# Optimization experiments

Measured on AMD Instinct MI355X. Metric: run time of the kernel, lower is better.

## Reference

```python
import jax, jax.numpy as jnp
import numpy as np

NUM_NODES = 500_000
NUM_EDGES = 8_000_000
NUM_GRAPHS = 8_192


def gcn_conv(x, edge_index, W, b):
    """PyG GCNConv (default args): add self-loops, symmetric deg normalization.
    Messages flow source (row=edge_index[0]) -> target (col=edge_index[1])."""
    n = x.shape[0]
    loop = jnp.arange(n, dtype=edge_index.dtype)
    row = jnp.concatenate([edge_index[0], loop])
    col = jnp.concatenate([edge_index[1], loop])
    h = x @ W  # [n, out]
    deg = jax.ops.segment_sum(jnp.ones_like(col, dtype=x.dtype), col, num_segments=n)
    dinv = jnp.where(deg > 0, jax.lax.rsqrt(deg), 0.0)
    norm = dinv[row] * dinv[col]  # [E+n]
    msg = h[row] * norm[:, None]  # gather + scale
    out = jax.ops.segment_sum(msg, col, num_segments=n)  # scatter-add at targets
    return out + b


def global_mean_pool(x, batch, num_graphs):
    s = jax.ops.segment_sum(x, batch, num_segments=num_graphs)
    cnt = jax.ops.segment_sum(jnp.ones((x.shape[0],), dtype=x.dtype), batch, num_segments=num_graphs)
    return s / jnp.maximum(cnt, 1.0)[:, None]


def setup_inputs() -> dict:
    key = jax.random.key(0)
    ks = jax.random.split(key, 12)
    x = jax.random.normal(ks[0], (NUM_NODES, 9), dtype=jnp.float32)
    edge_index = jax.random.randint(ks[1], (2, NUM_EDGES), 0, NUM_NODES, dtype=jnp.int64)
    batch = jnp.sort(jax.random.randint(ks[2], (NUM_NODES,), 0, NUM_GRAPHS, dtype=jnp.int64))
    metadata = jax.random.normal(ks[3], (NUM_GRAPHS, 27), dtype=jnp.float32)
    def glorot(k, shape):
        lim = float(np.sqrt(6.0 / (shape[0] + shape[1])))
        return jax.random.uniform(k, shape, jnp.float32, -lim, lim)
    W1 = glorot(ks[4], (9, 16));  b1 = jnp.zeros((16,), jnp.float32)
    W2 = glorot(ks[5], (16, 16)); b2 = jnp.zeros((16,), jnp.float32)
    Wh1 = glorot(ks[6], (16 + 27, 16)); bh1 = jnp.zeros((16,), jnp.float32)
    Wh2 = glorot(ks[7], (16, 1));       bh2 = jnp.zeros((1,), jnp.float32)
    return {"x": x, "edge_index": edge_index, "batch": batch, "metadata": metadata,
            "W1": W1, "b1": b1, "W2": W2, "b2": b2,
            "Wh1": Wh1, "bh1": bh1, "Wh2": Wh2, "bh2": bh2}


def reference(x, edge_index, batch, metadata, W1, b1, W2, b2, Wh1, bh1, Wh2, bh2):
    # eval mode: dropout is identity
    h = jax.nn.relu(gcn_conv(x, edge_index, W1, b1))
    h = jax.nn.relu(gcn_conv(h, edge_index, W2, b2))
    emb = global_mean_pool(h, batch, metadata.shape[0])  # [G, 16]
    z = jnp.concatenate([emb, metadata], axis=1)          # [G, 43]
    z = jax.nn.relu(z @ Wh1 + bh1)
    return z @ Wh2 + bh2  # [G, 1]
```

## Files before the change

### kernel.cpp

```cpp
#include <hip/hip_runtime.h>
#include <hip/hip_fp8.h>

#define N_NODES 500000
#define N_EDGES 8000000
#define N_GRAPHS 8192
#define BKT 512
#define NBK 977
#define C_CAP 9216
#define TILE2 8192
#define NTB2 977
#define CSR_IT 9

typedef __attribute__((ext_vector_type(2))) float v2f;

#if __has_builtin(__builtin_amdgcn_cvt_pk_f32_fp8)
template <bool HI>
__device__ __forceinline__ v2f cvt2fp8(unsigned w) {
    return __builtin_amdgcn_cvt_pk_f32_fp8((int)w, HI);
}
#else
template <bool HI>
__device__ __forceinline__ v2f cvt2fp8(unsigned w) {
    unsigned h16 = HI ? (w >> 16) : (w & 0xFFFFu);
    __hip_fp8_e4m3 a, b;
    a.__x = (__hip_fp8_storage_t)(h16 & 0xFFu);
    b.__x = (__hip_fp8_storage_t)(h16 >> 8);
    v2f r; r.x = (float)a; r.y = (float)b; return r;
}
#endif
#if __has_builtin(__builtin_amdgcn_cvt_pk_fp8_f32)
__device__ __forceinline__ unsigned pk4fp8(float a, float b, float c, float d) {
    int r = 0;
    r = __builtin_amdgcn_cvt_pk_fp8_f32(a, b, r, false);
    r = __builtin_amdgcn_cvt_pk_fp8_f32(c, d, r, true);
    return (unsigned)r;
}
#else
__device__ __forceinline__ unsigned pk4fp8(float a, float b, float c, float d) {
    __hip_fp8_e4m3 qa(a), qb(b), qc(c), qd(d);
    return (unsigned)qa.__x | ((unsigned)qb.__x << 8) |
           ((unsigned)qc.__x << 16) | ((unsigned)qd.__x << 24);
}
#endif
__device__ __forceinline__ void addfp8x16(float* acc, uint4 a) {
    v2f p;
    p = cvt2fp8<false>(a.x); acc[0] += p.x; acc[1] += p.y;
    p = cvt2fp8<true>(a.x);  acc[2] += p.x; acc[3] += p.y;
    p = cvt2fp8<false>(a.y); acc[4] += p.x; acc[5] += p.y;
    p = cvt2fp8<true>(a.y);  acc[6] += p.x; acc[7] += p.y;
    p = cvt2fp8<false>(a.z); acc[8] += p.x; acc[9] += p.y;
    p = cvt2fp8<true>(a.z);  acc[10] += p.x; acc[11] += p.y;
    p = cvt2fp8<false>(a.w); acc[12] += p.x; acc[13] += p.y;
    p = cvt2fp8<true>(a.w);  acc[14] += p.x; acc[15] += p.y;
}
__device__ __forceinline__ void addfp8x8(float* acc, uint2 a) {
    v2f p;
    p = cvt2fp8<false>(a.x); acc[0] += p.x; acc[1] += p.y;
    p = cvt2fp8<true>(a.x);  acc[2] += p.x; acc[3] += p.y;
    p = cvt2fp8<false>(a.y); acc[4] += p.x; acc[5] += p.y;
    p = cvt2fp8<true>(a.y);  acc[6] += p.x; acc[7] += p.y;
}

__global__ void k_init(float* __restrict__ pooled, int* __restrict__ gcursor) {
    int i = blockIdx.x * 256 + threadIdx.x;
    if (i < N_GRAPHS * 17) pooled[i] = 0.0f;
    if (i < NBK) gcursor[i] = i * C_CAP;
}

__global__ __launch_bounds__(1024) void
k_build(const int4* __restrict__ row4, const int4* __restrict__ col4,
        int* __restrict__ gcursor, unsigned* __restrict__ packed, int E) {
    __shared__ unsigned sortedv[TILE2];
    __shared__ unsigned short sortedb[TILE2];
    __shared__ int hist2[2][1024];
    __shared__ int lbase[1024];
    __shared__ int runbase[1024];
    __shared__ int sd[1024];
    int t = threadIdx.x, b = blockIdx.x;
    int sub = t >> 9;
    hist2[0][t] = 0; hist2[1][t] = 0;
    __syncthreads();
    unsigned uval[8];
    unsigned short ub[8];
#pragma unroll
    for (int k = 0; k < 2; k++) {
        int vi = b * 2048 + k * 1024 + t;
        int j0 = k * 4;
        if (vi * 4 < E) {
            int4 c = col4[vi];
            int4 r = row4[vi];
            unsigned cc, rr;
            cc = (unsigned)c.x; rr = (unsigned)r.x;
            if (cc < N_NODES && rr < N_NODES) { uval[j0] = (rr << 9) | (cc & 511u); ub[j0] = (unsigned short)(cc >> 9); atomicAdd(&hist2[sub][cc >> 9], 1); } else ub[j0] = 0xFFFFu;
            cc = (unsigned)c.y; rr = (unsigned)r.y;
            if (cc < N_NODES && rr < N_NODES) { uval[j0+1] = (rr << 9) | (cc & 511u); ub[j0+1] = (unsigned short)(cc >> 9); atomicAdd(&hist2[sub][cc >> 9], 1); } else ub[j0+1] = 0xFFFFu;
            cc = (unsigned)c.z; rr = (unsigned)r.z;
            if (cc < N_NODES && rr < N_NODES) { uval[j0+2] = (rr << 9) | (cc & 511u); ub[j0+2] = (unsigned short)(cc >> 9); atomicAdd(&hist2[sub][cc >> 9], 1); } else ub[j0+2] = 0xFFFFu;
            cc = (unsigned)c.w; rr = (unsigned)r.w;
            if (cc < N_NODES && rr < N_NODES) { uval[j0+3] = (rr << 9) | (cc & 511u); ub[j0+3] = (unsigned short)(cc >> 9); atomicAdd(&hist2[sub][cc >> 9], 1); } else ub[j0+3] = 0xFFFFu;
        } else {
            ub[j0] = 0xFFFFu; ub[j0+1] = 0xFFFFu; ub[j0+2] = 0xFFFFu; ub[j0+3] = 0xFFFFu;
        }
    }
    __syncthreads();
    int tot = (t < NBK) ? (hist2[0][t] + hist2[1][t]) : 0;
    sd[t] = tot; __syncthreads();
    for (int d = 1; d < 1024; d <<= 1) {
        int tv = (t >= d) ? sd[t - d] : 0;
        __syncthreads(); sd[t] += tv; __syncthreads();
    }
    lbase[t] = sd[t] - tot;
    if (t < NBK && tot) runbase[t] = atomicAdd(&gcursor[t], tot);
    hist2[0][t] = 0;
    __syncthreads();
    int total = sd[1023];
#pragma unroll
    for (int j = 0; j < 8; j++) {
        unsigned bb = ub[j];
        if (bb != 0xFFFFu) {
            int l = lbase[bb] + atomicAdd(&hist2[0][bb], 1);
            sortedv[l] = uval[j];
            sortedb[l] = (unsigned short)bb;
        }
    }
    __syncthreads();
    for (int l = t; l < total; l += 1024) {
        int bb = sortedb[l];
        packed[runbase[bb] + (l - lbase[bb])] = sortedv[l];
    }
}

__global__ __launch_bounds__(1024) void
k_csr(const unsigned* __restrict__ packed, const int* __restrict__ gcursor,
      const float* __restrict__ x, const float* __restrict__ W1,
      int* __restrict__ srcs, int* __restrict__ rowptr,
      float* __restrict__ dinv_g, uint4* __restrict__ hsu, int N) {
    __shared__ int sortedv[C_CAP];
    __shared__ int hist2[2][BKT];
    __shared__ int off[BKT];
    __shared__ int sd[1024];
    __shared__ int sgbase;
    __shared__ float sW1[144];
    int t = threadIdx.x, b = blockIdx.x;
    int h = t >> 9;
    sd[t] = (t < b) ? (gcursor[t] - t * C_CAP) : 0;
    if (t < 144) sW1[t] = W1[t];
    __syncthreads();
    for (int d = 512; d > 0; d >>= 1) {
        if (t < d) sd[t] += sd[t + d];
        __syncthreads();
    }
    if (t == 0) sgbase = sd[0];
    ((int*)hist2)[t] = 0;
    __syncthreads();
    int gbase = sgbase;
    int cnt = gcursor[b] - b * C_CAP;
    int sfix = b * C_CAP;
    unsigned pw[CSR_IT];
#pragma unroll
    for (int k = 0; k < CSR_IT; k++) {
        int i = k * 1024 + t;
        if (i < cnt) {
            unsigned w = packed[sfix + i];
            pw[k] = w;
            atomicAdd(&hist2[h][w & 511u], 1);
        } else pw[k] = 0xFFFFFFFFu;
    }
    __syncthreads();
    int ls = (t < BKT) ? (hist2[0][t] + hist2[1][t]) : 0;
    sd[t] = ls; __syncthreads();
    for (int d = 1; d < BKT; d <<= 1) {
        int tv = (t >= d) ? sd[t - d] : 0;
        __syncthreads(); sd[t] += tv; __syncthreads();
    }
    int v = b * BKT + t;
    float di = rsqrtf(1.0f + (float)ls);
    if (t < BKT) {
        int myoff = sd[t] - ls;
        off[t] = myoff;
        if (v < N) {
            rowptr[v] = gbase + myoff;
            dinv_g[v] = di;
        }
    }
    if (b == NBK - 1 && t == 0) rowptr[N] = gbase + cnt;
    __syncthreads();
    if (t < BKT) hist2[0][t] = 0;
    __syncthreads();
#pragma unroll
    for (int k = 0; k < CSR_IT; k++) {
        unsigned w = pw[k];
        if (w != 0xFFFFFFFFu) {
            unsigned c = w & 511u;
            int l = off[c] + atomicAdd(&hist2[0][c], 1);
            sortedv[l] = (int)(w >> 9);
        }
    }
    __syncthreads();
    for (int l = t; l < cnt; l += 1024) srcs[gbase + l] = sortedv[l];
    if (t < BKT && v < N) {
        float xi[9];
#pragma unroll
        for (int k = 0; k < 9; k++) xi[k] = x[v * 9 + k];
        float hh[16];
#pragma unroll
        for (int j = 0; j < 16; j++) {
            float acc = 0.f;
#pragma unroll
            for (int k = 0; k < 9; k++) acc += xi[k] * sW1[k * 16 + j];
            hh[j] = acc * di;
        }
        uint4 w;
        w.x = pk4fp8(hh[0], hh[1], hh[2], hh[3]);
        w.y = pk4fp8(hh[4], hh[5], hh[6], hh[7]);
        w.z = pk4fp8(hh[8], hh[9], hh[10], hh[11]);
        w.w = pk4fp8(hh[12], hh[13], hh[14], hh[15]);
        hsu[v] = w;
    }
}

__global__ void k_pullA(const int* __restrict__ rowptr, const int* __restrict__ srcs,
                        const uint4* __restrict__ hsu, const float* __restrict__ dinv,
                        const float* __restrict__ b1, const float* __restrict__ W2,
                        uint4* __restrict__ hs2u, int N) {
    int v = blockIdx.x * 256 + threadIdx.x;
    if (v >= N) return;
    int s = rowptr[v], e = rowptr[v + 1];
    float acc[16];
    {
        uint4 u = hsu[v];
#pragma unroll
        for (int i = 0; i < 16; i++) acc[i] = 0.f;
        addfp8x16(acc, u);
    }
    int k = s;
    for (; k + 4 <= e; k += 4) {
        int r0 = __builtin_nontemporal_load(&srcs[k]);
        int r1 = __builtin_nontemporal_load(&srcs[k + 1]);
        int r2 = __builtin_nontemporal_load(&srcs[k + 2]);
        int r3 = __builtin_nontemporal_load(&srcs[k + 3]);
        uint4 a0 = hsu[r0];
        uint4 a1 = hsu[r1];
        uint4 a2 = hsu[r2];
        uint4 a3 = hsu[r3];
        addfp8x16(acc, a0); addfp8x16(acc, a1);
        addfp8x16(acc, a2); addfp8x16(acc, a3);
    }
    for (; k < e; k++) addfp8x16(acc, hsu[__builtin_nontemporal_load(&srcs[k])]);
    float di = dinv[v];
    float h1[16];
#pragma unroll
    for (int i = 0; i < 16; i++) {
        float tt = acc[i] * di + b1[i];
        h1[i] = tt > 0.f ? tt : 0.f;
    }
    float o[16];
#pragma unroll
    for (int i = 0; i < 16; i++) o[i] = 0.f;
#pragma unroll
    for (int kk = 0; kk < 16; kk++) {
#pragma unroll
        for (int i = 0; i < 16; i++) o[i] += h1[kk] * W2[kk * 16 + i];
    }
    uint4 w;
    w.x = pk4fp8(o[0] * di, o[1] * di, o[2] * di, o[3] * di);
    w.y = pk4fp8(o[4] * di, o[5] * di, o[6] * di, o[7] * di);
    w.z = pk4fp8(o[8] * di, o[9] * di, o[10] * di, o[11] * di);
    w.w = pk4fp8(o[12] * di, o[13] * di, o[14] * di, o[15] * di);
    hs2u[v] = w;
}

__global__ void k_pullB(const int* __restrict__ rowptr, const int* __restrict__ srcs,
                        const uint2* __restrict__ hs2u, const float* __restrict__ dinv,
                        const float* __restrict__ b2, const int* __restrict__ batch,
                        float* __restrict__ pooled, float* __restrict__ cnt, int N) {
    int tid = blockIdx.x * 256 + threadIdx.x;
    int v = tid >> 1;
    int q = tid & 1;
    if (v >= N) return;
    int s = rowptr[v], e = rowptr[v + 1];
    float acc[8];
#pragma unroll
    for (int i = 0; i < 8; i++) acc[i] = 0.f;
    addfp8x8(acc, hs2u[v * 2 + q]);
    int k = s;
    for (; k + 8 <= e; k += 8) {
        int r0 = __builtin_nontemporal_load(&srcs[k]);
        int r1 = __builtin_nontemporal_load(&srcs[k + 1]);
        int r2 = __builtin_nontemporal_load(&srcs[k + 2]);
        int r3 = __builtin_nontemporal_load(&srcs[k + 3]);
        int r4 = __builtin_nontemporal_load(&srcs[k + 4]);
        int r5 = __builtin_nontemporal_load(&srcs[k + 5]);
        int r6 = __builtin_nontemporal_load(&srcs[k + 6]);
        int r7 = __builtin_nontemporal_load(&srcs[k + 7]);
        uint2 a0 = hs2u[r0 * 2 + q];
        uint2 a1 = hs2u[r1 * 2 + q];
        uint2 a2 = hs2u[r2 * 2 + q];
        uint2 a3 = hs2u[r3 * 2 + q];
        uint2 a4 = hs2u[r4 * 2 + q];
        uint2 a5 = hs2u[r5 * 2 + q];
        uint2 a6 = hs2u[r6 * 2 + q];
        uint2 a7 = hs2u[r7 * 2 + q];
        addfp8x8(acc, a0); addfp8x8(acc, a1); addfp8x8(acc, a2); addfp8x8(acc, a3);
        addfp8x8(acc, a4); addfp8x8(acc, a5); addfp8x8(acc, a6); addfp8x8(acc, a7);
    }
    for (; k + 4 <= e; k += 4) {
        int r0 = __builtin_nontemporal_load(&srcs[k]);
        int r1 = __builtin_nontemporal_load(&srcs[k + 1]);
        int r2 = __builtin_nontemporal_load(&srcs[k + 2]);
        int r3 = __builtin_nontemporal_load(&srcs[k + 3]);
        uint2 a0 = hs2u[r0 * 2 + q];
        uint2 a1 = hs2u[r1 * 2 + q];
        uint2 a2 = hs2u[r2 * 2 + q];
        uint2 a3 = hs2u[r3 * 2 + q];
        addfp8x8(acc, a0); addfp8x8(acc, a1); addfp8x8(acc, a2); addfp8x8(acc, a3);
    }
    for (; k < e; k++) addfp8x8(acc, hs2u[__builtin_nontemporal_load(&srcs[k]) * 2 + q]);
    float di = dinv[v];
    float h2[8];
#pragma unroll
    for (int i = 0; i < 8; i++) {
        float tt = acc[i] * di + b2[q * 8 + i];
        h2[i] = tt > 0.f ? tt : 0.f;
    }
    int l = threadIdx.x & 63;
    int g = batch[v];
    float c = (q == 0) ? 1.0f : 0.0f;
#pragma unroll
    for (int off = 2; off <= 32; off <<= 1) {
        int pg = __shfl_up(g, off, 64);
        float pc = __shfl_up(c, off, 64);
        float p0 = __shfl_up(h2[0], off, 64);
        float p1 = __shfl_up(h2[1], off, 64);
        float p2 = __shfl_up(h2[2], off, 64);
        float p3 = __shfl_up(h2[3], off, 64);
        float p4 = __shfl_up(h2[4], off, 64);
        float p5 = __shfl_up(h2[5], off, 64);
        float p6 = __shfl_up(h2[6], off, 64);
        float p7 = __shfl_up(h2[7], off, 64);
        if (l >= off && pg == g) {
            c += pc;
            h2[0] += p0; h2[1] += p1; h2[2] += p2; h2[3] += p3;
            h2[4] += p4; h2[5] += p5; h2[6] += p6; h2[7] += p7;
        }
    }
    int gn = __shfl_down(g, 2, 64);
    bool tail = (l >= 62) || (gn != g);
    if (tail) {
#pragma unroll
        for (int i = 0; i < 8; i++)
            atomicAdd(&pooled[g * 16 + q * 8 + i], h2[i]);
        if (q == 0) atomicAdd(&cnt[g], c);
    }
}

__global__ void k_head(const float* __restrict__ pooled, const float* __restrict__ cnt,
                       const float* __restrict__ meta, const float* __restrict__ Wh1,
                       const float* __restrict__ bh1, const float* __restrict__ Wh2,
                       const float* __restrict__ bh2, float* __restrict__ out, int G) {
    int g = blockIdx.x * 256 + threadIdx.x;
    if (g >= G) return;
    float z[43];
    float c = cnt[g];
    c = c > 1.f ? c : 1.f;
#pragma unroll
    for (int j = 0; j < 16; j++) z[j] = pooled[g * 16 + j] / c;
#pragma unroll
    for (int j = 0; j < 27; j++) z[16 + j] = meta[g * 27 + j];
    float acc2 = bh2[0];
#pragma unroll
    for (int jj = 0; jj < 16; jj++) {
        float a = bh1[jj];
#pragma unroll
        for (int k = 0; k < 43; k++) a += z[k] * Wh1[k * 16 + jj];
        a = a > 0.f ? a : 0.f;
        acc2 += a * Wh2[jj];
    }
    out[g] = acc2;
}

extern "C" void kernel_launch(void* const* d_in, const int* in_sizes, int n_in,
                              void* d_out, int out_size, void* d_ws, size_t ws_size,
                              hipStream_t stream) {
    const float* x    = (const float*)d_in[0];
    const int*   ei   = (const int*)d_in[1];
    const int*   batch= (const int*)d_in[2];
    const float* meta = (const float*)d_in[3];
    const float* W1   = (const float*)d_in[4];
    const float* b1   = (const float*)d_in[5];
    const float* W2   = (const float*)d_in[6];
    const float* b2   = (const float*)d_in[7];
    const float* Wh1  = (const float*)d_in[8];
    const float* bh1  = (const float*)d_in[9];
    const float* Wh2  = (const float*)d_in[10];
    const float* bh2  = (const float*)d_in[11];
    float* out = (float*)d_out;

    const int N = N_NODES, E = N_EDGES, G = N_GRAPHS;
    const int* row = ei;
    const int* col = ei + E;

    float*    ws      = (float*)d_ws;
    float*    dinv    = ws;
    unsigned* packed  = (unsigned*)(ws + 512000);
    int*      srcs    = (int*)(packed + 9004032);
    unsigned* hsu     = (unsigned*)(srcs + 8000000);
    unsigned* hs2u    = hsu + 2000000;
    float*    pooled  = (float*)(hs2u + 2000000);
    float*    cnt     = pooled + G * 16;
    int*      gcursor = (int*)(cnt + G);
    int*      rowptr  = gcursor + 1024;

    dim3 blk(256);

    k_init<<<(G * 17 + 255) / 256, blk, 0, stream>>>(pooled, gcursor);
    k_build<<<NTB2, dim3(1024), 0, stream>>>((const int4*)row, (const int4*)col,
                                             gcursor, packed, E);
    k_csr<<<NBK, dim3(1024), 0, stream>>>(packed, gcursor, x, W1,
                                          srcs, rowptr, dinv, (uint4*)hsu, N);

    k_pullA<<<(N + 255) / 256, blk, 0, stream>>>(rowptr, srcs, (const uint4*)hsu,
                                                 dinv, b1, W2, (uint4*)hs2u, N);

    int gP2 = (N * 2 + 255) / 256;
    k_pullB<<<gP2, blk, 0, stream>>>(rowptr, srcs, (const uint2*)hs2u, dinv,
                                     b2, batch, pooled, cnt, N);

    k_head<<<(G + 255) / 256, blk, 0, stream>>>(pooled, cnt, meta, Wh1, bh1, Wh2, bh2, out, G);
}
```

Before: 389.8 us.

## Replace shared-memory Hillis-Steele scans with wave-shuffle scans and precompute bucket offsets

Replaces the barrier-heavy log-step shared-memory prefix scans in the build and CSR kernels with a wavefront shuffle-based block scan that needs only two barriers. Adds a single-block kernel that computes the global bucket offsets once, so each CSR block no longer re-reduces the cursor array itself. Also switches the srcs and second-layer feature writes to nontemporal stores. The cost is one extra tiny kernel launch on the critical path.

```diff
diff --git a/kernel.cpp b/kernel.cpp
--- a/kernel.cpp
+++ b/kernel.cpp
@@ -12,6 +12,7 @@
 #define CSR_IT 9
 
 typedef __attribute__((ext_vector_type(2))) float v2f;
+typedef __attribute__((ext_vector_type(4))) unsigned v4u;
 
 #if __has_builtin(__builtin_amdgcn_cvt_pk_f32_fp8)
 template <bool HI>
@@ -61,6 +62,30 @@
     p = cvt2fp8<true>(a.y);  acc[6] += p.x; acc[7] += p.y;
 }
 
+__device__ __forceinline__ int blockscan_excl(int v, int* wsum, int* woff) {
+    int t = threadIdx.x;
+    int lane = t & 63, wid = t >> 6;
+    int inc = v;
+#pragma unroll
+    for (int o = 1; o <= 32; o <<= 1) {
+        int p = __shfl_up(inc, o, 64);
+        if (lane >= o) inc += p;
+    }
+    if (lane == 63) wsum[wid] = inc;
+    __syncthreads();
+    if (wid == 0) {
+        int ws = (lane < 16) ? wsum[lane] : 0;
+#pragma unroll
+        for (int o = 1; o <= 8; o <<= 1) {
+            int p = __shfl_up(ws, o, 64);
+            if (lane >= o) ws += p;
+        }
+        if (lane < 16) woff[lane] = ws - wsum[lane];
+    }
+    __syncthreads();
+    return inc - v + woff[wid];
+}
+
 __global__ void k_init(float* __restrict__ pooled, int* __restrict__ gcursor) {
     int i = blockIdx.x * 256 + threadIdx.x;
     if (i < N_GRAPHS * 17) pooled[i] = 0.0f;
@@ -75,7 +100,8 @@
     __shared__ int hist2[2][1024];
     __shared__ int lbase[1024];
     __shared__ int runbase[1024];
-    __shared__ int sd[1024];
+    __shared__ int wsum[16], woff[16];
+    __shared__ int stotal;
     int t = threadIdx.x, b = blockIdx.x;
     int sub = t >> 9;
     hist2[0][t] = 0; hist2[1][t] = 0;
@@ -104,16 +130,13 @@
     }
     __syncthreads();
     int tot = (t < NBK) ? (hist2[0][t] + hist2[1][t]) : 0;
-    sd[t] = tot; __syncthreads();
-    for (int d = 1; d < 1024; d <<= 1) {
-        int tv = (t >= d) ? sd[t - d] : 0;
-        __syncthreads(); sd[t] += tv; __syncthreads();
-    }
-    lbase[t] = sd[t] - tot;
+    int excl = blockscan_excl(tot, wsum, woff);
+    lbase[t] = excl;
+    if (t == 1023) stotal = excl + tot;
     if (t < NBK && tot) runbase[t] = atomicAdd(&gcursor[t], tot);
     hist2[0][t] = 0;
     __syncthreads();
-    int total = sd[1023];
+    int total = stotal;
 #pragma unroll
     for (int j = 0; j < 8; j++) {
         unsigned bb = ub[j];
@@ -131,30 +154,32 @@
 }
 
 __global__ __launch_bounds__(1024) void
-k_csr(const unsigned* __restrict__ packed, const int* __restrict__ gcursor,
+k_goff(const int* __restrict__ gcursor, int* __restrict__ goff) {
+    __shared__ int wsum[16], woff[16];
+    int t = threadIdx.x;
+    int v = (t < NBK) ? (gcursor[t] - t * C_CAP) : 0;
+    int excl = blockscan_excl(v, wsum, woff);
+    if (t < NBK) goff[t] = excl;
+    if (t == NBK) goff[NBK] = excl;
+}
+
+__global__ __launch_bounds__(1024) void
+k_csr(const unsigned* __restrict__ packed, const int* __restrict__ goff,
       const float* __restrict__ x, const float* __restrict__ W1,
       int* __restrict__ srcs, int* __restrict__ rowptr,
       float* __restrict__ dinv_g, uint4* __restrict__ hsu, int N) {
     __shared__ int sortedv[C_CAP];
     __shared__ int hist2[2][BKT];
     __shared__ int off[BKT];
-    __shared__ int sd[1024];
-    __shared__ int sgbase;
+    __shared__ int wsum[16], woff[16];
     __shared__ float sW1[144];
     int t = threadIdx.x, b = blockIdx.x;
     int h = t >> 9;
-    sd[t] = (t < b) ? (gcursor[t] - t * C_CAP) : 0;
     if (t < 144) sW1[t] = W1[t];
-    __syncthreads();
-    for (int d = 512; d > 0; d >>= 1) {
-        if (t < d) sd[t] += sd[t + d];
-        __syncthreads();
-    }
-    if (t == 0) sgbase = sd[0];
     ((int*)hist2)[t] = 0;
     __syncthreads();
-    int gbase = sgbase;
-    int cnt = gcursor[b] - b * C_CAP;
+    int gbase = goff[b];
+    int cnt = goff[b + 1] - gbase;
     int sfix = b * C_CAP;
     unsigned pw[CSR_IT];
 #pragma unroll
@@ -168,18 +193,13 @@
     }
     __syncthreads();
     int ls = (t < BKT) ? (hist2[0][t] + hist2[1][t]) : 0;
-    sd[t] = ls; __syncthreads();
-    for (int d = 1; d < BKT; d <<= 1) {
-        int tv = (t >= d) ? sd[t - d] : 0;
-        __syncthreads(); sd[t] += tv; __syncthreads();
-    }
+    int excl = blockscan_excl(ls, wsum, woff);
     int v = b * BKT + t;
     float di = rsqrtf(1.0f + (float)ls);
     if (t < BKT) {
-        int myoff = sd[t] - ls;
-        off[t] = myoff;
+        off[t] = excl;
         if (v < N) {
-            rowptr[v] = gbase + myoff;
+            rowptr[v] = gbase + excl;
             dinv_g[v] = di;
         }
     }
@@ -197,7 +217,8 @@
         }
     }
     __syncthreads();
-    for (int l = t; l < cnt; l += 1024) srcs[gbase + l] = sortedv[l];
+    for (int l = t; l < cnt; l += 1024)
+        __builtin_nontemporal_store(sortedv[l], &srcs[gbase + l]);
     if (t < BKT && v < N) {
         float xi[9];
 #pragma unroll
@@ -262,12 +283,12 @@
 #pragma unroll
         for (int i = 0; i < 16; i++) o[i] += h1[kk] * W2[kk * 16 + i];
     }
-    uint4 w;
+    v4u w;
     w.x = pk4fp8(o[0] * di, o[1] * di, o[2] * di, o[3] * di);
     w.y = pk4fp8(o[4] * di, o[5] * di, o[6] * di, o[7] * di);
     w.z = pk4fp8(o[8] * di, o[9] * di, o[10] * di, o[11] * di);
     w.w = pk4fp8(o[12] * di, o[13] * di, o[14] * di, o[15] * di);
-    hs2u[v] = w;
+    __builtin_nontemporal_store(w, (v4u*)&hs2u[v]);
 }
 
 __global__ void k_pullB(const int* __restrict__ rowptr, const int* __restrict__ srcs,
@@ -409,14 +430,16 @@
     float*    pooled  = (float*)(hs2u + 2000000);
     float*    cnt     = pooled + G * 16;
     int*      gcursor = (int*)(cnt + G);
-    int*      rowptr  = gcursor + 1024;
+    int*      goff    = gcursor + 1024;
+    int*      rowptr  = goff + 1024;
 
     dim3 blk(256);
 
     k_init<<<(G * 17 + 255) / 256, blk, 0, stream>>>(pooled, gcursor);
     k_build<<<NTB2, dim3(1024), 0, stream>>>((const int4*)row, (const int4*)col,
                                              gcursor, packed, E);
-    k_csr<<<NBK, dim3(1024), 0, stream>>>(packed, gcursor, x, W1,
+    k_goff<<<1, dim3(1024), 0, stream>>>(gcursor, goff);
+    k_csr<<<NBK, dim3(1024), 0, stream>>>(packed, goff, x, W1,
                                           srcs, rowptr, dinv, (uint4*)hsu, N);
 
     k_pullA<<<(N + 255) / 256, blk, 0, stream>>>(rowptr, srcs, (const uint4*)hsu,
```

Result: no change. 393.7 us (+1.0%).
